# Kernel tuning notes

Measured on AMD Instinct MI355X. Metric: run time of the kernel, lower is better.

The kernel has to match this reference:

```python
import jax, jax.numpy as jnp
import numpy as np

B, S, D_IN, D_MODEL, H = 4, 2048, 1024, 1024, 16
HD = D_MODEL // H  # 64


def setup_inputs() -> dict:
    key = jax.random.key(0)
    k1, k2, k3, k4, k5 = jax.random.split(key, 5)
    x = jax.random.normal(k1, (B, S, D_IN), dtype=jnp.float32)
    mask = jnp.zeros((1, 1, S, S), dtype=jnp.float32)  # additive mask
    # qkv_layer: Linear(D_IN, 3*D_MODEL)
    W_qkv = jax.random.normal(k2, (D_IN, 3 * D_MODEL), dtype=jnp.float32) / np.sqrt(D_IN)
    b_qkv = jax.random.normal(k3, (3 * D_MODEL,), dtype=jnp.float32) * 0.01
    # linear_layer: Linear(D_MODEL, D_MODEL)
    W_o = jax.random.normal(k4, (D_MODEL, D_MODEL), dtype=jnp.float32) / np.sqrt(D_MODEL)
    b_o = jax.random.normal(k5, (D_MODEL,), dtype=jnp.float32) * 0.01
    return {"x": x, "mask": mask, "W_qkv": W_qkv, "b_qkv": b_qkv, "W_o": W_o, "b_o": b_o}


def reference(x, mask, W_qkv, b_qkv, W_o, b_o):
    b, s, _ = x.shape
    qkv = x @ W_qkv + b_qkv                                  # [B,S,3*D]
    qkv = qkv.reshape(b, s, H, 3 * HD).transpose(0, 2, 1, 3)  # [B,H,S,3*HD]
    q, k, v = jnp.split(qkv, 3, axis=-1)                     # each [B,H,S,HD]
    scale = 1.0 / jnp.sqrt(jnp.asarray(HD, dtype=q.dtype))
    scores = jnp.einsum('bhqd,bhkd->bhqk', q, k) * scale + mask  # [B,H,S,S]
    attn = jax.nn.softmax(scores, axis=-1)
    values = jnp.einsum('bhqk,bhkd->bhqd', attn, v)           # [B,H,S,HD]
    values = values.transpose(0, 2, 1, 3).reshape(b, s, H * HD)  # [B,S,D]
    out = values @ W_o + b_o
    return (out, values)
```

## Files before the change

### kernel.cpp

```cpp
#include <hip/hip_runtime.h>
#include <hip/hip_bf16.h>


typedef __attribute__((ext_vector_type(8))) short short8;
typedef __attribute__((ext_vector_type(4))) float f32x4;

#define GLD16(g, l)                                                            \
  __builtin_amdgcn_global_load_lds(                                            \
      (const __attribute__((address_space(1))) unsigned int*)(g),              \
      (__attribute__((address_space(3))) unsigned int*)(l), 16, 0, 0)

__device__ __forceinline__ unsigned short f2b(float f) {
  union { float f; unsigned int u; } v; v.f = f;
  unsigned int u = v.u;
  return (unsigned short)((u + 0x7fffu + ((u >> 16) & 1u)) >> 16);
}
__device__ __forceinline__ unsigned int fbits(float f) {
  union { float f; unsigned int u; } v; v.f = f; return v.u;
}
__device__ __forceinline__ float bfloat(unsigned int u) {
  union { float f; unsigned int u; } v; v.u = u; return v.f;
}

__global__ void cvt_bf16(const float* __restrict__ in, ushort* __restrict__ out, int n) {
  int i = (blockIdx.x * blockDim.x + threadIdx.x) * 4;
  if (i + 3 < n) {
    float4 f = *(const float4*)(in + i);
    ushort4 o;
    o.x = f2b(f.x); o.y = f2b(f.y); o.z = f2b(f.z); o.w = f2b(f.w);
    *(ushort4*)(out + i) = o;
  }
}

__global__ void transpose_cvt(const float* __restrict__ W, ushort* __restrict__ Wt,
                              int K, int N) {
  __shared__ float tile[64][65];
  int n0 = blockIdx.x * 64, k0 = blockIdx.y * 64;
  int tx = threadIdx.x & 63, ty = threadIdx.x >> 6;
#pragma unroll
  for (int i = 0; i < 64; i += 4)
    tile[ty + i][tx] = W[(size_t)(k0 + ty + i) * N + n0 + tx];
  __syncthreads();
#pragma unroll
  for (int i = 0; i < 64; i += 4)
    Wt[(size_t)(n0 + ty + i) * K + k0 + tx] = f2b(tile[tx][ty + i]);
}

template <int OUTF32>
__global__ __launch_bounds__(256, 2) void gemm_bt_bias(
    const ushort* __restrict__ A, const ushort* __restrict__ Bt,
    const float* __restrict__ bias, void* __restrict__ Cout,
    int M, int N, int K) {
  __shared__ ushort As[128 * 64];
  __shared__ ushort Bs[128 * 64];
  const int lane = threadIdx.x & 63;
  const int wv = threadIdx.x >> 6;
  const int bm = blockIdx.y, bn = blockIdx.x;
  const int wm = wv >> 1, wn = wv & 1;
  f32x4 acc[4][4] = {};
  const size_t arow0 = (size_t)bm * 128;
  const size_t brow0 = (size_t)bn * 128;

  for (int k0 = 0; k0 < K; k0 += 64) {
    __syncthreads();
#pragma unroll
    for (int i = 0; i < 4; ++i) {
      int r = wv * 32 + i * 8 + (lane >> 3);
      const ushort* ga = A + (arow0 + r) * K + k0 + (lane & 7) * 8;
      GLD16(ga, As + (wv * 32 + i * 8) * 64);
      const ushort* gb = Bt + (brow0 + r) * K + k0 + (lane & 7) * 8;
      GLD16(gb, Bs + (wv * 32 + i * 8) * 64);
    }
    __syncthreads();
    short8 af[2][4], bf[2][4];
#pragma unroll
    for (int kf = 0; kf < 2; ++kf)
#pragma unroll
      for (int t = 0; t < 4; ++t) {
        af[kf][t] = *(const short8*)(As + (wm * 64 + t * 16 + (lane & 15)) * 64 +
                                     kf * 32 + (lane >> 4) * 8);
        bf[kf][t] = *(const short8*)(Bs + (wn * 64 + t * 16 + (lane & 15)) * 64 +
                                     kf * 32 + (lane >> 4) * 8);
      }
#pragma unroll
    for (int kf = 0; kf < 2; ++kf)
#pragma unroll
      for (int mt = 0; mt < 4; ++mt)
#pragma unroll
        for (int nt = 0; nt < 4; ++nt)
          acc[mt][nt] = __builtin_amdgcn_mfma_f32_16x16x32_bf16(
              af[kf][mt], bf[kf][nt], acc[mt][nt], 0, 0, 0);
  }
#pragma unroll
  for (int nt = 0; nt < 4; ++nt) {
    int col = bn * 128 + wn * 64 + nt * 16 + (lane & 15);
    float bv = bias[col];
#pragma unroll
    for (int mt = 0; mt < 4; ++mt) {
      int row0 = bm * 128 + wm * 64 + mt * 16 + (lane >> 4) * 4;
#pragma unroll
      for (int r = 0; r < 4; ++r) {
        float v = acc[mt][nt][r] + bv;
        if (OUTF32)
          ((float*)Cout)[(size_t)(row0 + r) * N + col] = v;
        else
          ((ushort*)Cout)[(size_t)(row0 + r) * N + col] = f2b(v);
      }
    }
  }
}

#define SCL2E 0.1803368801111204f
#define L2E   1.44269504088896340736f

__global__ __launch_bounds__(256, 2) void flash_attn(
    const ushort* __restrict__ qkv, const float* __restrict__ mask,
    float* __restrict__ values_f, ushort* __restrict__ values_b) {
  __shared__ ushort Ks[2][128 * 64];
  __shared__ ushort Vt[2][64 * 136];

  const int lane = threadIdx.x & 63;
  const int wv = threadIdx.x >> 6;
  const int c = lane & 15;
  const int g = lane >> 4;
  const int bh = blockIdx.x & 63;
  const int qt = blockIdx.x >> 6;
  const int b = bh >> 4, h = bh & 15;
  const size_t rowbase = (size_t)b * 2048;
  const int qcol = h * 192;
  const int swz = (c & 3) << 1;

  short8 qf[2][2];
#pragma unroll
  for (int mt = 0; mt < 2; ++mt)
#pragma unroll
    for (int kf = 0; kf < 2; ++kf)
      qf[mt][kf] = *(const short8*)(qkv +
          (rowbase + qt * 128 + wv * 32 + mt * 16 + c) * 3072 + qcol +
          kf * 32 + g * 8);

  f32x4 acc[2][4] = {};
  float mst[2] = {-3e38f, -3e38f}, lst[2] = {0.f, 0.f};

  const int kp = threadIdx.x & 63, dq = threadIdx.x >> 6;
  const int K0 = kp * 2;
  const int pc0 = ((K0 >> 5) << 5) + (((K0 >> 2) & 3) << 3) +
                  (((K0 >> 4) & 1) << 2) + (K0 & 3);
  const int vdw = pc0 >> 1;
  const int gcol = (((lane & 7) ^ (((lane >> 3) & 3) << 1)) << 3);

  short8 va0, va1, vb0, vb1;

  auto loadV = [&](int t) {
    const ushort* vg = qkv + (rowbase + t * 128 + K0) * 3072 + qcol + 128 + dq * 16;
    va0 = *(const short8*)(vg);
    va1 = *(const short8*)(vg + 8);
    vb0 = *(const short8*)(vg + 3072);
    vb1 = *(const short8*)(vg + 3072 + 8);
  };
  auto writeV = [&](ushort* VtD) {
    unsigned int* Vdw = (unsigned int*)VtD;
#pragma unroll
    for (int j = 0; j < 8; ++j)
      Vdw[(dq * 16 + j) * 68 + vdw] =
          ((unsigned int)(unsigned short)vb0[j] << 16) | (unsigned short)va0[j];
#pragma unroll
    for (int j = 0; j < 8; ++j)
      Vdw[(dq * 16 + 8 + j) * 68 + vdw] =
          ((unsigned int)(unsigned short)vb1[j] << 16) | (unsigned short)va1[j];
  };
  auto stageK = [&](int t, ushort* KsD) {
#pragma unroll
    for (int i = 0; i < 4; ++i) {
      int rloc = wv * 32 + i * 8;
      const ushort* gk = qkv + (rowbase + t * 128 + rloc + (lane >> 3)) * 3072 +
                         qcol + 64 + gcol;
      GLD16(gk, KsD + rloc * 64);
    }
  };

  const float* mrow = mask + (size_t)(qt * 128 + wv * 32 + c) * 2048 + g * 4;

  loadV(0);
  stageK(0, Ks[0]);
  writeV(Vt[0]);
  __syncthreads();

  for (int kt = 0; kt < 16; ++kt) {
    const int cur = kt & 1;
    const ushort* KsC = Ks[cur];
    const ushort* VtC = Vt[cur];
    if (kt < 15) {
      loadV(kt + 1);
      stageK(kt + 1, Ks[cur ^ 1]);
    }

    const float* mkt = mrow + kt * 128;
    float4 msk0[8];
#pragma unroll
    for (int nt = 0; nt < 8; ++nt) msk0[nt] = *(const float4*)(mkt + nt * 16);

    f32x4 sc[2][8];
    __builtin_amdgcn_s_setprio(1);
#pragma unroll
    for (int nt = 0; nt < 8; ++nt) {
      short8 k0 = *(const short8*)(KsC + (nt * 16 + c) * 64 + ((g ^ swz) << 3));
      short8 k1 = *(const short8*)(KsC + (nt * 16 + c) * 64 + (((4 + g) ^ swz) << 3));
      f32x4 z = {0.f, 0.f, 0.f, 0.f};
      sc[0][nt] = __builtin_amdgcn_mfma_f32_16x16x32_bf16(k0, qf[0][0], z, 0, 0, 0);
      sc[0][nt] = __builtin_amdgcn_mfma_f32_16x16x32_bf16(k1, qf[0][1], sc[0][nt], 0, 0, 0);
      sc[1][nt] = __builtin_amdgcn_mfma_f32_16x16x32_bf16(k0, qf[1][0], z, 0, 0, 0);
      sc[1][nt] = __builtin_amdgcn_mfma_f32_16x16x32_bf16(k1, qf[1][1], sc[1][nt], 0, 0, 0);
    }
    __builtin_amdgcn_s_setprio(0);

    __attribute__((aligned(16))) unsigned int Dw[2][16];
#pragma unroll
    for (int mt = 0; mt < 2; ++mt) {
      f32x4 t4[8];
#pragma unroll
      for (int nt = 0; nt < 8; ++nt) {
        float4 mk = (mt == 0) ? msk0[nt]
                              : *(const float4*)(mkt + 16 * 2048 + nt * 16);
#pragma unroll
        for (int r = 0; r < 4; ++r)
          t4[nt][r] = sc[mt][nt][r] * SCL2E + ((const float*)&mk)[r] * L2E;
      }
      f32x4 vm = t4[0];
#pragma unroll
      for (int nt = 1; nt < 8; ++nt)
#pragma unroll
        for (int r = 0; r < 4; ++r) vm[r] = fmaxf(vm[r], t4[nt][r]);
      float pm = fmaxf(fmaxf(vm[0], vm[1]), fmaxf(vm[2], vm[3]));
      pm = fmaxf(pm, __shfl_xor(pm, 16));
      pm = fmaxf(pm, __shfl_xor(pm, 32));
      if (!__all(pm <= mst[mt] + 8.0f)) {
        float mnew = fmaxf(mst[mt], pm);
        float alpha = exp2f(mst[mt] - mnew);
        mst[mt] = mnew;
        lst[mt] *= alpha;
#pragma unroll
        for (int dt = 0; dt < 4; ++dt)
#pragma unroll
          for (int r = 0; r < 4; ++r) acc[mt][dt][r] *= alpha;
      }
      const float mcur = mst[mt];
      f32x4 rsv = {0.f, 0.f, 0.f, 0.f};
#pragma unroll
      for (int nt = 0; nt < 8; ++nt) {
        unsigned int pu[4];
#pragma unroll
        for (int r = 0; r < 4; ++r) {
          float p = exp2f(t4[nt][r] - mcur);
          pu[r] = fbits(p) & 0xffff0000u;
          rsv[r] += bfloat(pu[r]);
        }
        Dw[mt][nt * 2 + 0] = pu[1] | (pu[0] >> 16);
        Dw[mt][nt * 2 + 1] = pu[3] | (pu[2] >> 16);
      }
      float rs = (rsv[0] + rsv[1]) + (rsv[2] + rsv[3]);
      rs += __shfl_xor(rs, 16);
      rs += __shfl_xor(rs, 32);
      lst[mt] += rs;
    }

    const short8* bu0 = (const short8*)Dw[0];
    const short8* bu1 = (const short8*)Dw[1];
    __builtin_amdgcn_s_setprio(1);
#pragma unroll
    for (int dt = 0; dt < 4; ++dt)
#pragma unroll
      for (int kf = 0; kf < 4; ++kf) {
        short8 vf = *(const short8*)(VtC + (dt * 16 + c) * 136 + kf * 32 + g * 8);
        acc[0][dt] = __builtin_amdgcn_mfma_f32_16x16x32_bf16(vf, bu0[kf], acc[0][dt], 0, 0, 0);
        acc[1][dt] = __builtin_amdgcn_mfma_f32_16x16x32_bf16(vf, bu1[kf], acc[1][dt], 0, 0, 0);
      }
    __builtin_amdgcn_s_setprio(0);

    if (kt < 15) writeV(Vt[cur ^ 1]);
    __syncthreads();
  }

#pragma unroll
  for (int mt = 0; mt < 2; ++mt) {
    float rl = 1.0f / lst[mt];
    size_t qrow = rowbase + qt * 128 + wv * 32 + mt * 16 + c;
#pragma unroll
    for (int dt = 0; dt < 4; ++dt) {
      int d0 = h * 64 + dt * 16 + g * 4;
      float4 o;
      o.x = acc[mt][dt][0] * rl; o.y = acc[mt][dt][1] * rl;
      o.z = acc[mt][dt][2] * rl; o.w = acc[mt][dt][3] * rl;
      *(float4*)(values_f + qrow * 1024 + d0) = o;
      ushort4 ob;
      ob.x = f2b(o.x); ob.y = f2b(o.y); ob.z = f2b(o.z); ob.w = f2b(o.w);
      *(ushort4*)(values_b + qrow * 1024 + d0) = ob;
    }
  }
}

extern "C" void kernel_launch(void* const* d_in, const int* in_sizes, int n_in,
                              void* d_out, int out_size, void* d_ws, size_t ws_size,
                              hipStream_t stream) {
  const float* x    = (const float*)d_in[0];
  const float* mask = (const float*)d_in[1];
  const float* Wqkv = (const float*)d_in[2];
  const float* bqkv = (const float*)d_in[3];
  const float* Wo   = (const float*)d_in[4];
  const float* bo   = (const float*)d_in[5];
  float* out      = (float*)d_out;
  float* values_f = out + 8388608;

  char* ws = (char*)d_ws;
  ushort* xb    = (ushort*)(ws + 0);
  ushort* wqkvt = (ushort*)(ws + 16777216);
  ushort* wot   = (ushort*)(ws + 23068672);
  ushort* qkv   = (ushort*)(ws + 25165824);
  ushort* valb  = (ushort*)(ws + 75497472);

  cvt_bf16<<<dim3(8192), dim3(256), 0, stream>>>(x, xb, 8388608);
  transpose_cvt<<<dim3(48, 16), dim3(256), 0, stream>>>(Wqkv, wqkvt, 1024, 3072);
  transpose_cvt<<<dim3(16, 16), dim3(256), 0, stream>>>(Wo, wot, 1024, 1024);
  gemm_bt_bias<0><<<dim3(24, 64), dim3(256), 0, stream>>>(
      xb, wqkvt, bqkv, (void*)qkv, 8192, 3072, 1024);
  flash_attn<<<dim3(1024), dim3(256), 0, stream>>>(qkv, mask, values_f, valb);
  gemm_bt_bias<1><<<dim3(8, 64), dim3(256), 0, stream>>>(
      valb, wot, bo, (void*)out, 8192, 1024, 1024);
}
```

Measured before the change: 430.9 us.

## Make flash attention persistent with atomic work queue and single V buffer

Turns flash_attn into a persistent kernel of 768 blocks that pull (batch, head, q-tile) work items from an atomic counter, which is reset inside cvt_bf16. V is now single-buffered, with an extra barrier before each V write, to cut LDS use and allow 3 blocks per CU. The softmax scale is folded into Q in the QKV GEMM epilogue, and the packed bf16 conversion uses v_cvt_pk_bf16_f32 instead of truncation. The aim is better occupancy and less per-tile ALU work, at the cost of an extra sync per K tile and a serialized atomic per work item.

```diff
diff --git a/kernel.cpp b/kernel.cpp
--- a/kernel.cpp
+++ b/kernel.cpp
@@ -4,6 +4,9 @@
 
 typedef __attribute__((ext_vector_type(8))) short short8;
 typedef __attribute__((ext_vector_type(4))) float f32x4;
+
+#define SCL2E 0.1803368801111204f
+#define L2E   1.44269504088896340736f
 
 #define GLD16(g, l)                                                            \
   __builtin_amdgcn_global_load_lds(                                            \
@@ -15,14 +18,15 @@
   unsigned int u = v.u;
   return (unsigned short)((u + 0x7fffu + ((u >> 16) & 1u)) >> 16);
 }
-__device__ __forceinline__ unsigned int fbits(float f) {
-  union { float f; unsigned int u; } v; v.f = f; return v.u;
-}
-__device__ __forceinline__ float bfloat(unsigned int u) {
-  union { float f; unsigned int u; } v; v.u = u; return v.f;
-}
-
-__global__ void cvt_bf16(const float* __restrict__ in, ushort* __restrict__ out, int n) {
+__device__ __forceinline__ unsigned int cvt_pk_bf16(float lo, float hi) {
+  unsigned int r;
+  asm("v_cvt_pk_bf16_f32 %0, %1, %2" : "=v"(r) : "v"(lo), "v"(hi));
+  return r;
+}
+
+__global__ void cvt_bf16(const float* __restrict__ in, ushort* __restrict__ out,
+                         int n, unsigned int* __restrict__ wcnt) {
+  if (blockIdx.x == 0 && threadIdx.x == 0) *wcnt = 0u;
   int i = (blockIdx.x * blockDim.x + threadIdx.x) * 4;
   if (i + 3 < n) {
     float4 f = *(const float4*)(in + i);
@@ -46,7 +50,7 @@
     Wt[(size_t)(n0 + ty + i) * K + k0 + tx] = f2b(tile[tx][ty + i]);
 }
 
-template <int OUTF32>
+template <int OUTF32, int QSCALE>
 __global__ __launch_bounds__(256, 2) void gemm_bt_bias(
     const ushort* __restrict__ A, const ushort* __restrict__ Bt,
     const float* __restrict__ bias, void* __restrict__ Cout,
@@ -95,12 +99,14 @@
   for (int nt = 0; nt < 4; ++nt) {
     int col = bn * 128 + wn * 64 + nt * 16 + (lane & 15);
     float bv = bias[col];
+    float scl = (QSCALE && (col % 192) < 64) ? SCL2E : 1.0f;
 #pragma unroll
     for (int mt = 0; mt < 4; ++mt) {
       int row0 = bm * 128 + wm * 64 + mt * 16 + (lane >> 4) * 4;
 #pragma unroll
       for (int r = 0; r < 4; ++r) {
         float v = acc[mt][nt][r] + bv;
+        if (QSCALE) v *= scl;
         if (OUTF32)
           ((float*)Cout)[(size_t)(row0 + r) * N + col] = v;
         else
@@ -110,40 +116,22 @@
   }
 }
 
-#define SCL2E 0.1803368801111204f
-#define L2E   1.44269504088896340736f
-
-__global__ __launch_bounds__(256, 2) void flash_attn(
+__global__ __launch_bounds__(256, 3) void flash_attn(
     const ushort* __restrict__ qkv, const float* __restrict__ mask,
-    float* __restrict__ values_f, ushort* __restrict__ values_b) {
+    float* __restrict__ values_f, ushort* __restrict__ values_b,
+    unsigned int* __restrict__ wcnt) {
   __shared__ ushort Ks[2][128 * 64];
-  __shared__ ushort Vt[2][64 * 136];
+  __shared__ ushort Vt[64 * 136];
+  __shared__ int wslot;
 
   const int lane = threadIdx.x & 63;
   const int wv = threadIdx.x >> 6;
   const int c = lane & 15;
   const int g = lane >> 4;
-  const int bh = blockIdx.x & 63;
-  const int qt = blockIdx.x >> 6;
-  const int b = bh >> 4, h = bh & 15;
-  const size_t rowbase = (size_t)b * 2048;
-  const int qcol = h * 192;
   const int swz = (c & 3) << 1;
 
-  short8 qf[2][2];
-#pragma unroll
-  for (int mt = 0; mt < 2; ++mt)
-#pragma unroll
-    for (int kf = 0; kf < 2; ++kf)
-      qf[mt][kf] = *(const short8*)(qkv +
-          (rowbase + qt * 128 + wv * 32 + mt * 16 + c) * 3072 + qcol +
-          kf * 32 + g * 8);
-
-  f32x4 acc[2][4] = {};
-  float mst[2] = {-3e38f, -3e38f}, lst[2] = {0.f, 0.f};
-
-  const int kp = threadIdx.x & 63, dq = threadIdx.x >> 6;
-  const int K0 = kp * 2;
+  const int K0 = lane * 2;
+  const int dq = wv;
   const int pc0 = ((K0 >> 5) << 5) + (((K0 >> 2) & 3) << 3) +
                   (((K0 >> 4) & 1) << 2) + (K0 & 3);
   const int vdw = pc0 >> 1;
@@ -151,15 +139,15 @@
 
   short8 va0, va1, vb0, vb1;
 
-  auto loadV = [&](int t) {
+  auto loadV = [&](size_t rowbase, int qcol, int t) {
     const ushort* vg = qkv + (rowbase + t * 128 + K0) * 3072 + qcol + 128 + dq * 16;
     va0 = *(const short8*)(vg);
     va1 = *(const short8*)(vg + 8);
     vb0 = *(const short8*)(vg + 3072);
     vb1 = *(const short8*)(vg + 3072 + 8);
   };
-  auto writeV = [&](ushort* VtD) {
-    unsigned int* Vdw = (unsigned int*)VtD;
+  auto writeV = [&]() {
+    unsigned int* Vdw = (unsigned int*)Vt;
 #pragma unroll
     for (int j = 0; j < 8; ++j)
       Vdw[(dq * 16 + j) * 68 + vdw] =
@@ -169,7 +157,7 @@
       Vdw[(dq * 16 + 8 + j) * 68 + vdw] =
           ((unsigned int)(unsigned short)vb1[j] << 16) | (unsigned short)va1[j];
   };
-  auto stageK = [&](int t, ushort* KsD) {
+  auto stageK = [&](size_t rowbase, int qcol, int t, ushort* KsD) {
 #pragma unroll
     for (int i = 0; i < 4; ++i) {
       int rloc = wv * 32 + i * 8;
@@ -179,122 +167,144 @@
     }
   };
 
-  const float* mrow = mask + (size_t)(qt * 128 + wv * 32 + c) * 2048 + g * 4;
-
-  loadV(0);
-  stageK(0, Ks[0]);
-  writeV(Vt[0]);
-  __syncthreads();
-
-  for (int kt = 0; kt < 16; ++kt) {
-    const int cur = kt & 1;
-    const ushort* KsC = Ks[cur];
-    const ushort* VtC = Vt[cur];
-    if (kt < 15) {
-      loadV(kt + 1);
-      stageK(kt + 1, Ks[cur ^ 1]);
-    }
-
-    const float* mkt = mrow + kt * 128;
-    float4 msk0[8];
-#pragma unroll
-    for (int nt = 0; nt < 8; ++nt) msk0[nt] = *(const float4*)(mkt + nt * 16);
-
-    f32x4 sc[2][8];
-    __builtin_amdgcn_s_setprio(1);
-#pragma unroll
-    for (int nt = 0; nt < 8; ++nt) {
-      short8 k0 = *(const short8*)(KsC + (nt * 16 + c) * 64 + ((g ^ swz) << 3));
-      short8 k1 = *(const short8*)(KsC + (nt * 16 + c) * 64 + (((4 + g) ^ swz) << 3));
-      f32x4 z = {0.f, 0.f, 0.f, 0.f};
-      sc[0][nt] = __builtin_amdgcn_mfma_f32_16x16x32_bf16(k0, qf[0][0], z, 0, 0, 0);
-      sc[0][nt] = __builtin_amdgcn_mfma_f32_16x16x32_bf16(k1, qf[0][1], sc[0][nt], 0, 0, 0);
-      sc[1][nt] = __builtin_amdgcn_mfma_f32_16x16x32_bf16(k0, qf[1][0], z, 0, 0, 0);
-      sc[1][nt] = __builtin_amdgcn_mfma_f32_16x16x32_bf16(k1, qf[1][1], sc[1][nt], 0, 0, 0);
-    }
-    __builtin_amdgcn_s_setprio(0);
-
-    __attribute__((aligned(16))) unsigned int Dw[2][16];
+  for (;;) {
+    if (threadIdx.x == 0) wslot = (int)atomicAdd(wcnt, 1u);
+    __syncthreads();
+    const int u = wslot;
+    if (u >= 1024) break;
+    const int bh = u & 63;
+    const int qt = u >> 6;
+    const int b = bh >> 4, h = bh & 15;
+    const size_t rowbase = (size_t)b * 2048;
+    const int qcol = h * 192;
+
+    short8 qf[2][2];
+#pragma unroll
+    for (int mt = 0; mt < 2; ++mt)
+#pragma unroll
+      for (int kf = 0; kf < 2; ++kf)
+        qf[mt][kf] = *(const short8*)(qkv +
+            (rowbase + qt * 128 + wv * 32 + mt * 16 + c) * 3072 + qcol +
+            kf * 32 + g * 8);
+
+    f32x4 acc[2][4] = {};
+    float mst[2] = {-3e38f, -3e38f}, lst[2] = {0.f, 0.f};
+    const float* mrow = mask + (size_t)(qt * 128 + wv * 32 + c) * 2048 + g * 4;
+
+    loadV(rowbase, qcol, 0);
+    stageK(rowbase, qcol, 0, Ks[0]);
+    writeV();
+
+    for (int kt = 0; kt < 16; ++kt) {
+      __syncthreads();
+      const int cur = kt & 1;
+      const ushort* KsC = Ks[cur];
+      if (kt < 15) {
+        loadV(rowbase, qcol, kt + 1);
+        stageK(rowbase, qcol, kt + 1, Ks[cur ^ 1]);
+      }
+
+      const float* mkt = mrow + kt * 128;
+      float4 msk0[8];
+#pragma unroll
+      for (int nt = 0; nt < 8; ++nt) msk0[nt] = *(const float4*)(mkt + nt * 16);
+
+      f32x4 sc[2][8];
+      __builtin_amdgcn_s_setprio(1);
+#pragma unroll
+      for (int nt = 0; nt < 8; ++nt) {
+        short8 k0 = *(const short8*)(KsC + (nt * 16 + c) * 64 + ((g ^ swz) << 3));
+        short8 k1 = *(const short8*)(KsC + (nt * 16 + c) * 64 + (((4 + g) ^ swz) << 3));
+        f32x4 z = {0.f, 0.f, 0.f, 0.f};
+        sc[0][nt] = __builtin_amdgcn_mfma_f32_16x16x32_bf16(k0, qf[0][0], z, 0, 0, 0);
+        sc[0][nt] = __builtin_amdgcn_mfma_f32_16x16x32_bf16(k1, qf[0][1], sc[0][nt], 0, 0, 0);
+        sc[1][nt] = __builtin_amdgcn_mfma_f32_16x16x32_bf16(k0, qf[1][0], z, 0, 0, 0);
+        sc[1][nt] = __builtin_amdgcn_mfma_f32_16x16x32_bf16(k1, qf[1][1], sc[1][nt], 0, 0, 0);
+      }
+      __builtin_amdgcn_s_setprio(0);
+
+      __attribute__((aligned(16))) unsigned int Dw[2][16];
+#pragma unroll
+      for (int mt = 0; mt < 2; ++mt) {
+        f32x4 t4[8];
+#pragma unroll
+        for (int nt = 0; nt < 8; ++nt) {
+          float4 mk = (mt == 0) ? msk0[nt]
+                                : *(const float4*)(mkt + 16 * 2048 + nt * 16);
+#pragma unroll
+          for (int r = 0; r < 4; ++r)
+            t4[nt][r] = fmaf(((const float*)&mk)[r], L2E, sc[mt][nt][r]);
+        }
+        f32x4 vm = t4[0];
+#pragma unroll
+        for (int nt = 1; nt < 8; ++nt)
+#pragma unroll
+          for (int r = 0; r < 4; ++r) vm[r] = fmaxf(vm[r], t4[nt][r]);
+        float pm = fmaxf(fmaxf(vm[0], vm[1]), fmaxf(vm[2], vm[3]));
+        pm = fmaxf(pm, __shfl_xor(pm, 16));
+        pm = fmaxf(pm, __shfl_xor(pm, 32));
+        if (!__all(pm <= mst[mt] + 8.0f)) {
+          float mnew = fmaxf(mst[mt], pm);
+          float alpha = exp2f(mst[mt] - mnew);
+          mst[mt] = mnew;
+          lst[mt] *= alpha;
+#pragma unroll
+          for (int dt = 0; dt < 4; ++dt)
+#pragma unroll
+            for (int r = 0; r < 4; ++r) acc[mt][dt][r] *= alpha;
+        }
+        const float mcur = mst[mt];
+        f32x4 rsv = {0.f, 0.f, 0.f, 0.f};
+#pragma unroll
+        for (int nt = 0; nt < 8; ++nt) {
+          float p0 = exp2f(t4[nt][0] - mcur);
+          float p1 = exp2f(t4[nt][1] - mcur);
+          float p2 = exp2f(t4[nt][2] - mcur);
+          float p3 = exp2f(t4[nt][3] - mcur);
+          rsv[0] += p0; rsv[1] += p1; rsv[2] += p2; rsv[3] += p3;
+          Dw[mt][nt * 2 + 0] = cvt_pk_bf16(p0, p1);
+          Dw[mt][nt * 2 + 1] = cvt_pk_bf16(p2, p3);
+        }
+        float rs = (rsv[0] + rsv[1]) + (rsv[2] + rsv[3]);
+        rs += __shfl_xor(rs, 16);
+        rs += __shfl_xor(rs, 32);
+        lst[mt] += rs;
+      }
+
+      const short8* bu0 = (const short8*)Dw[0];
+      const short8* bu1 = (const short8*)Dw[1];
+      __builtin_amdgcn_s_setprio(1);
+#pragma unroll
+      for (int dt = 0; dt < 4; ++dt)
+#pragma unroll
+        for (int kf = 0; kf < 4; ++kf) {
+          short8 vf = *(const short8*)(Vt + (dt * 16 + c) * 136 + kf * 32 + g * 8);
+          acc[0][dt] = __builtin_amdgcn_mfma_f32_16x16x32_bf16(vf, bu0[kf], acc[0][dt], 0, 0, 0);
+          acc[1][dt] = __builtin_amdgcn_mfma_f32_16x16x32_bf16(vf, bu1[kf], acc[1][dt], 0, 0, 0);
+        }
+      __builtin_amdgcn_s_setprio(0);
+
+      if (kt < 15) {
+        __syncthreads();
+        writeV();
+      }
+    }
+
 #pragma unroll
     for (int mt = 0; mt < 2; ++mt) {
-      f32x4 t4[8];
-#pragma unroll
-      for (int nt = 0; nt < 8; ++nt) {
-        float4 mk = (mt == 0) ? msk0[nt]
-                              : *(const float4*)(mkt + 16 * 2048 + nt * 16);
-#pragma unroll
-        for (int r = 0; r < 4; ++r)
-          t4[nt][r] = sc[mt][nt][r] * SCL2E + ((const float*)&mk)[r] * L2E;
-      }
-      f32x4 vm = t4[0];
-#pragma unroll
-      for (int nt = 1; nt < 8; ++nt)
-#pragma unroll
-        for (int r = 0; r < 4; ++r) vm[r] = fmaxf(vm[r], t4[nt][r]);
-      float pm = fmaxf(fmaxf(vm[0], vm[1]), fmaxf(vm[2], vm[3]));
-      pm = fmaxf(pm, __shfl_xor(pm, 16));
-      pm = fmaxf(pm, __shfl_xor(pm, 32));
-      if (!__all(pm <= mst[mt] + 8.0f)) {
-        float mnew = fmaxf(mst[mt], pm);
-        float alpha = exp2f(mst[mt] - mnew);
-        mst[mt] = mnew;
-        lst[mt] *= alpha;
-#pragma unroll
-        for (int dt = 0; dt < 4; ++dt)
-#pragma unroll
-          for (int r = 0; r < 4; ++r) acc[mt][dt][r] *= alpha;
-      }
-      const float mcur = mst[mt];
-      f32x4 rsv = {0.f, 0.f, 0.f, 0.f};
-#pragma unroll
-      for (int nt = 0; nt < 8; ++nt) {
-        unsigned int pu[4];
-#pragma unroll
-        for (int r = 0; r < 4; ++r) {
-          float p = exp2f(t4[nt][r] - mcur);
-          pu[r] = fbits(p) & 0xffff0000u;
-          rsv[r] += bfloat(pu[r]);
-        }
-        Dw[mt][nt * 2 + 0] = pu[1] | (pu[0] >> 16);
-        Dw[mt][nt * 2 + 1] = pu[3] | (pu[2] >> 16);
-      }
-      float rs = (rsv[0] + rsv[1]) + (rsv[2] + rsv[3]);
-      rs += __shfl_xor(rs, 16);
-      rs += __shfl_xor(rs, 32);
-      lst[mt] += rs;
-    }
-
-    const short8* bu0 = (const short8*)Dw[0];
-    const short8* bu1 = (const short8*)Dw[1];
-    __builtin_amdgcn_s_setprio(1);
-#pragma unroll
-    for (int dt = 0; dt < 4; ++dt)
-#pragma unroll
-      for (int kf = 0; kf < 4; ++kf) {
-        short8 vf = *(const short8*)(VtC + (dt * 16 + c) * 136 + kf * 32 + g * 8);
-        acc[0][dt] = __builtin_amdgcn_mfma_f32_16x16x32_bf16(vf, bu0[kf], acc[0][dt], 0, 0, 0);
-        acc[1][dt] = __builtin_amdgcn_mfma_f32_16x16x32_bf16(vf, bu1[kf], acc[1][dt], 0, 0, 0);
-      }
-    __builtin_amdgcn_s_setprio(0);
-
-    if (kt < 15) writeV(Vt[cur ^ 1]);
-    __syncthreads();
-  }
-
-#pragma unroll
-  for (int mt = 0; mt < 2; ++mt) {
-    float rl = 1.0f / lst[mt];
-    size_t qrow = rowbase + qt * 128 + wv * 32 + mt * 16 + c;
-#pragma unroll
-    for (int dt = 0; dt < 4; ++dt) {
-      int d0 = h * 64 + dt * 16 + g * 4;
-      float4 o;
-      o.x = acc[mt][dt][0] * rl; o.y = acc[mt][dt][1] * rl;
-      o.z = acc[mt][dt][2] * rl; o.w = acc[mt][dt][3] * rl;
-      *(float4*)(values_f + qrow * 1024 + d0) = o;
-      ushort4 ob;
-      ob.x = f2b(o.x); ob.y = f2b(o.y); ob.z = f2b(o.z); ob.w = f2b(o.w);
-      *(ushort4*)(values_b + qrow * 1024 + d0) = ob;
+      float rl = 1.0f / lst[mt];
+      size_t qrow = rowbase + qt * 128 + wv * 32 + mt * 16 + c;
+#pragma unroll
+      for (int dt = 0; dt < 4; ++dt) {
+        int d0 = h * 64 + dt * 16 + g * 4;
+        float4 o;
+        o.x = acc[mt][dt][0] * rl; o.y = acc[mt][dt][1] * rl;
+        o.z = acc[mt][dt][2] * rl; o.w = acc[mt][dt][3] * rl;
+        *(float4*)(values_f + qrow * 1024 + d0) = o;
+        ushort4 ob;
+        ob.x = f2b(o.x); ob.y = f2b(o.y); ob.z = f2b(o.z); ob.w = f2b(o.w);
+        *(ushort4*)(values_b + qrow * 1024 + d0) = ob;
+      }
     }
   }
 }
@@ -317,13 +327,14 @@
   ushort* wot   = (ushort*)(ws + 23068672);
   ushort* qkv   = (ushort*)(ws + 25165824);
   ushort* valb  = (ushort*)(ws + 75497472);
-
-  cvt_bf16<<<dim3(8192), dim3(256), 0, stream>>>(x, xb, 8388608);
+  unsigned int* wcnt = (unsigned int*)(ws + 92274688);
+
+  cvt_bf16<<<dim3(8192), dim3(256), 0, stream>>>(x, xb, 8388608, wcnt);
   transpose_cvt<<<dim3(48, 16), dim3(256), 0, stream>>>(Wqkv, wqkvt, 1024, 3072);
   transpose_cvt<<<dim3(16, 16), dim3(256), 0, stream>>>(Wo, wot, 1024, 1024);
-  gemm_bt_bias<0><<<dim3(24, 64), dim3(256), 0, stream>>>(
+  gemm_bt_bias<0, 1><<<dim3(24, 64), dim3(256), 0, stream>>>(
       xb, wqkvt, bqkv, (void*)qkv, 8192, 3072, 1024);
-  flash_attn<<<dim3(1024), dim3(256), 0, stream>>>(qkv, mask, values_f, valb);
-  gemm_bt_bias<1><<<dim3(8, 64), dim3(256), 0, stream>>>(
+  flash_attn<<<dim3(768), dim3(256), 0, stream>>>(qkv, mask, values_f, valb, wcnt);
+  gemm_bt_bias<1, 0><<<dim3(8, 64), dim3(256), 0, stream>>>(
       valb, wot, bo, (void*)out, 8192, 1024, 1024);
 }
```

Result: slower. 638.0 us (+48.0%).
